# Kernel tuning notes

Measured on AMD Instinct MI355X. Metric: run time of the kernel, lower is better.

Reference implementation:

```python
import jax, jax.numpy as jnp
import numpy as np

B, N, D_IN = 128, 128, 1024
H1, D_OUT = 256, 32
K = 8  # num_clusters


def setup_inputs() -> dict:
    key = jax.random.key(0)
    ks = jax.random.split(key, 3)
    x = jax.random.normal(ks[0], (B, N, D_IN), dtype=jnp.float32)
    W1 = jax.random.normal(ks[1], (D_IN, H1), dtype=jnp.float32) * (1.0 / np.sqrt(D_IN))
    b1 = jnp.zeros((H1,), jnp.float32)
    W2 = jax.random.normal(ks[2], (H1, D_OUT), dtype=jnp.float32) * (1.0 / np.sqrt(H1))
    b2 = jnp.zeros((D_OUT,), jnp.float32)
    return {"x": x, "W1": W1, "b1": b1, "W2": W2, "b2": b2}


def _mlp(x, W1, b1, W2, b2):
    # nn.Sequential(GELU, Linear(1024,256), GELU, Linear(256,32)); torch GELU default = exact erf
    h = jax.nn.gelu(x, approximate=False)
    h = h @ W1 + b1
    h = jax.nn.gelu(h, approximate=False)
    return h @ W2 + b2  # [B, N, 32]


def _ward_labels(feats, k):
    """Greedy ward-linkage agglomerative clustering of feats [n, d] -> int labels [n].
    Ward merge cost d(A,B) = |A||B|/(|A|+|B|) * ||c_A - c_B||^2 (Lance-Williams equiv)."""
    n = feats.shape[0]
    eye = jnp.eye(n, dtype=bool)

    def body(t, state):
        cents, sizes, lab = state
        sq = jnp.sum(cents * cents, axis=-1)
        d2 = jnp.maximum(sq[:, None] + sq[None, :] - 2.0 * (cents @ cents.T), 0.0)
        w = (sizes[:, None] * sizes[None, :]) / (sizes[:, None] + sizes[None, :] + 1e-30)
        active = sizes > 0
        valid = (active[:, None] & active[None, :]) & (~eye)
        Dm = jnp.where(valid, w * d2, jnp.inf)
        idx = jnp.argmin(Dm)
        i, j = idx // n, idx % n
        i2 = jnp.minimum(i, j)
        j2 = jnp.maximum(i, j)
        si, sj = sizes[i2], sizes[j2]
        newc = (cents[i2] * si + cents[j2] * sj) / (si + sj)
        cents = cents.at[i2].set(newc)
        sizes = sizes.at[i2].set(si + sj).at[j2].set(0.0)
        lab = jnp.where(lab == j2, i2, lab)
        return cents, sizes, lab

    init = (feats, jnp.ones((n,), feats.dtype), jnp.arange(n))
    cents, sizes, lab = jax.lax.fori_loop(0, n - k, body, init)
    # relabel surviving representative indices to 0..k-1 (ordered by index)
    rank = jnp.cumsum((sizes > 0).astype(jnp.int32)) - 1
    return rank[lab]


def reference(x, W1, b1, W2, b2):
    feats = _mlp(x, W1, b1, W2, b2)          # [B, N, 32]
    labels = jax.vmap(lambda f: _ward_labels(f, K))(feats)  # [B, N] int32
    return labels
```

## Files before the change

### kernel.cpp

```cpp
#include <hip/hip_runtime.h>
#include <math.h>

#define BB 128
#define NN 128
#define DIN 1024
#define H1 256
#define DOUT 32
#define KCL 8
#define NPTS 128
#define MROWS (BB*NN)
#define CSTR 130
#define RSTR 132
#define HSTR 257
#define DEADKEY 0xFFFFFFFF00000000ull

__device__ __forceinline__ float gelu_exact(float v) {
    return 0.5f * v * (1.0f + erff(v * 0.70710678118654752f));
}

__device__ __forceinline__ unsigned long long mkkey(float v, int r, int j) {
    return ((unsigned long long)__float_as_uint(v) << 32) | (unsigned)((r << 7) | j);
}

__device__ __forceinline__ float readlanef(float v, int lane) {
    return __int_as_float(__builtin_amdgcn_readlane(__float_as_int(v), lane));
}

template<int CTRL, int RMASK>
__device__ __forceinline__ unsigned dpp_umin_step(unsigned v) {
    unsigned t = (unsigned)__builtin_amdgcn_update_dpp((int)v, (int)v, CTRL, RMASK, 0xf, false);
    return t < v ? t : v;
}
__device__ __forceinline__ unsigned wave_umin_bcast(unsigned v) {
    v = dpp_umin_step<0x111, 0xf>(v);
    v = dpp_umin_step<0x112, 0xf>(v);
    v = dpp_umin_step<0x114, 0xf>(v);
    v = dpp_umin_step<0x118, 0xf>(v);
    v = dpp_umin_step<0x142, 0xa>(v);
    v = dpp_umin_step<0x143, 0xc>(v);
    return (unsigned)__builtin_amdgcn_readlane((int)v, 63);
}
__device__ __forceinline__ unsigned half_umin(unsigned v) {
    v = dpp_umin_step<0x111, 0xf>(v);
    v = dpp_umin_step<0x112, 0xf>(v);
    v = dpp_umin_step<0x114, 0xf>(v);
    v = dpp_umin_step<0x118, 0xf>(v);
    v = dpp_umin_step<0x142, 0xa>(v);
    return v;
}

__global__ __launch_bounds__(256) void gelu_kernel(const float* __restrict__ x,
                                                   float* __restrict__ gx, int n4) {
    int i = blockIdx.x * 256 + threadIdx.x;
    const int stride = gridDim.x * 256;
    for (; i < n4; i += stride) {
        float4 v = ((const float4*)x)[i];
        v.x = gelu_exact(v.x);
        v.y = gelu_exact(v.y);
        v.z = gelu_exact(v.z);
        v.w = gelu_exact(v.w);
        ((float4*)gx)[i] = v;
    }
}

template<bool FUSE>
__global__ __launch_bounds__(256) void mlp1_kernel(const float* __restrict__ xin,
                                                   const float* __restrict__ W1,
                                                   const float* __restrict__ b1,
                                                   float* __restrict__ h) {
    __shared__ float As[64][68];
    __shared__ float Bs[64][68];
    const int bn = blockIdx.x;
    const int bm = blockIdx.y;
    const int tid = threadIdx.x;
    const int tx = tid & 15, ty = tid >> 4;

    float acc[4][4] = {{0.f}};

    const int arow = tid >> 2;
    const int kc   = (tid & 3) * 4;
    const int brow = tid >> 4;
    const int bcol4 = (tid & 15) * 4;

    const float* xrow = xin + (size_t)(bm * 64 + arow) * DIN;
    const float* wbase = W1 + bn * 64;

    for (int kt = 0; kt < DIN; kt += 64) {
        float4 a0 = *(const float4*)(xrow + kt + kc);
        float4 a1 = *(const float4*)(xrow + kt + kc + 16);
        float4 a2 = *(const float4*)(xrow + kt + kc + 32);
        float4 a3 = *(const float4*)(xrow + kt + kc + 48);
        float4 w0 = *(const float4*)(wbase + (size_t)(kt + brow) * H1 + bcol4);
        float4 w1 = *(const float4*)(wbase + (size_t)(kt + 16 + brow) * H1 + bcol4);
        float4 w2 = *(const float4*)(wbase + (size_t)(kt + 32 + brow) * H1 + bcol4);
        float4 w3 = *(const float4*)(wbase + (size_t)(kt + 48 + brow) * H1 + bcol4);
        __syncthreads();
        if (FUSE) {
            As[kc + 0][arow] = gelu_exact(a0.x);
            As[kc + 1][arow] = gelu_exact(a0.y);
            As[kc + 2][arow] = gelu_exact(a0.z);
            As[kc + 3][arow] = gelu_exact(a0.w);
            As[16 + kc + 0][arow] = gelu_exact(a1.x);
            As[16 + kc + 1][arow] = gelu_exact(a1.y);
            As[16 + kc + 2][arow] = gelu_exact(a1.z);
            As[16 + kc + 3][arow] = gelu_exact(a1.w);
            As[32 + kc + 0][arow] = gelu_exact(a2.x);
            As[32 + kc + 1][arow] = gelu_exact(a2.y);
            As[32 + kc + 2][arow] = gelu_exact(a2.z);
            As[32 + kc + 3][arow] = gelu_exact(a2.w);
            As[48 + kc + 0][arow] = gelu_exact(a3.x);
            As[48 + kc + 1][arow] = gelu_exact(a3.y);
            As[48 + kc + 2][arow] = gelu_exact(a3.z);
            As[48 + kc + 3][arow] = gelu_exact(a3.w);
        } else {
            As[kc + 0][arow] = a0.x;
            As[kc + 1][arow] = a0.y;
            As[kc + 2][arow] = a0.z;
            As[kc + 3][arow] = a0.w;
            As[16 + kc + 0][arow] = a1.x;
            As[16 + kc + 1][arow] = a1.y;
            As[16 + kc + 2][arow] = a1.z;
            As[16 + kc + 3][arow] = a1.w;
            As[32 + kc + 0][arow] = a2.x;
            As[32 + kc + 1][arow] = a2.y;
            As[32 + kc + 2][arow] = a2.z;
            As[32 + kc + 3][arow] = a2.w;
            As[48 + kc + 0][arow] = a3.x;
            As[48 + kc + 1][arow] = a3.y;
            As[48 + kc + 2][arow] = a3.z;
            As[48 + kc + 3][arow] = a3.w;
        }
        *(float4*)&Bs[brow][bcol4] = w0;
        *(float4*)&Bs[16 + brow][bcol4] = w1;
        *(float4*)&Bs[32 + brow][bcol4] = w2;
        *(float4*)&Bs[48 + brow][bcol4] = w3;
        __syncthreads();
#pragma unroll
        for (int kk = 0; kk < 64; ++kk) {
            float4 a = *(const float4*)&As[kk][ty * 4];
            float4 b = *(const float4*)&Bs[kk][tx * 4];
            float ar[4] = {a.x, a.y, a.z, a.w};
            float br[4] = {b.x, b.y, b.z, b.w};
#pragma unroll
            for (int i = 0; i < 4; ++i)
#pragma unroll
                for (int j = 0; j < 4; ++j)
                    acc[i][j] = fmaf(ar[i], br[j], acc[i][j]);
        }
    }

    const int row = bm * 64 + ty * 4;
    const int col = bn * 64 + tx * 4;
    float4 bias = *(const float4*)(b1 + col);
#pragma unroll
    for (int i = 0; i < 4; ++i) {
        float4 o;
        o.x = acc[i][0] + bias.x;
        o.y = acc[i][1] + bias.y;
        o.z = acc[i][2] + bias.z;
        o.w = acc[i][3] + bias.w;
        *(float4*)(h + (size_t)(row + i) * H1 + col) = o;
    }
}

__global__ __launch_bounds__(256) void mlp2_kernel(const float* __restrict__ h,
                                                   const float* __restrict__ W2,
                                                   const float* __restrict__ b2,
                                                   float* __restrict__ feats) {
    __shared__ float hs[32 * HSTR];
    __shared__ float w2s[H1 * DOUT];
    const int blk = blockIdx.x;
    const int tid = threadIdx.x;

    for (int i = tid; i < (H1 * DOUT) / 4; i += 256)
        ((float4*)w2s)[i] = ((const float4*)W2)[i];

    const float* hb = h + (size_t)blk * 32 * H1;
    const int sr = tid & 31;
    const int sk = (tid >> 5) * 32;
    const float* hrow = hb + (size_t)sr * H1 + sk;
#pragma unroll
    for (int j = 0; j < 8; ++j) {
        float4 v = ((const float4*)hrow)[j];
        hs[sr * HSTR + sk + 4 * j + 0] = gelu_exact(v.x);
        hs[sr * HSTR + sk + 4 * j + 1] = gelu_exact(v.y);
        hs[sr * HSTR + sk + 4 * j + 2] = gelu_exact(v.z);
        hs[sr * HSTR + sk + 4 * j + 3] = gelu_exact(v.w);
    }
    __syncthreads();

    const int row = tid >> 3;
    const int col4 = (tid & 7) * 4;
    const float4 bias = ((const float4*)b2)[tid & 7];
    float a0 = 0.f, a1 = 0.f, a2 = 0.f, a3 = 0.f;
    const float* hr = &hs[row * HSTR];
    for (int k = 0; k < H1; ++k) {
        float a = hr[k];
        float4 w = *(const float4*)&w2s[k * DOUT + col4];
        a0 = fmaf(a, w.x, a0);
        a1 = fmaf(a, w.y, a1);
        a2 = fmaf(a, w.z, a2);
        a3 = fmaf(a, w.w, a3);
    }
    float4 o;
    o.x = a0 + bias.x;
    o.y = a1 + bias.y;
    o.z = a2 + bias.z;
    o.w = a3 + bias.w;
    *(float4*)(feats + (size_t)(blk * 32 + row) * DOUT + col4) = o;
}

__global__ __launch_bounds__(256) void ward_kernel(const float* __restrict__ feats,
                                                   int* __restrict__ out) {
    __shared__ __align__(16) float cost[NPTS * RSTR];
    __shared__ __align__(16) float G[NPTS * RSTR];
    __shared__ float centsT[32 * CSTR];
    __shared__ unsigned long long rowkey[NPTS];
    __shared__ float sqArr[NPTS];
    __shared__ float szsE[NPTS];
    __shared__ int rnk[NPTS];

    const int b = blockIdx.x;
    const int tid = threadIdx.x;
    const float* f = feats + (size_t)b * NPTS * DOUT;
    const float INF = __builtin_inff();

    for (int i = tid; i < NPTS * DOUT; i += 256) {
        int r = i >> 5, d = i & 31;
        centsT[d * CSTR + r] = f[i];
    }
    __syncthreads();
    if (tid < NPTS) {
        float s = 0.f;
#pragma unroll
        for (int d = 0; d < 32; ++d) {
            float v = centsT[d * CSTR + tid];
            s = fmaf(v, v, s);
        }
        sqArr[tid] = s;
    }
    __syncthreads();
    {
        int ti = tid >> 4, tj = tid & 15;
        int I0 = ti * 8, J0 = tj * 8;
        float acc[8][8];
#pragma unroll
        for (int u = 0; u < 8; ++u)
#pragma unroll
            for (int v = 0; v < 8; ++v) acc[u][v] = 0.f;
        for (int d = 0; d < 32; ++d) {
            float a[8], bb[8];
#pragma unroll
            for (int u = 0; u < 8; ++u) a[u] = centsT[d * CSTR + I0 + u];
#pragma unroll
            for (int v = 0; v < 8; ++v) bb[v] = centsT[d * CSTR + J0 + v];
#pragma unroll
            for (int u = 0; u < 8; ++u)
#pragma unroll
                for (int v = 0; v < 8; ++v)
                    acc[u][v] = fmaf(a[u], bb[v], acc[u][v]);
        }
#pragma unroll
        for (int u = 0; u < 8; ++u) {
#pragma unroll
            for (int v = 0; v < 8; ++v) {
                int i = I0 + u, j = J0 + v;
                G[i * RSTR + j] = acc[u][v];
                float d2 = sqArr[i] + sqArr[j] - 2.0f * acc[u][v];
                if (d2 < 0.f) d2 = 0.f;
                float w = (1.0f * 1.0f) / (1.0f + 1.0f + 1e-30f);
                cost[i * RSTR + j] = (i == j) ? INF : w * d2;
            }
        }
    }
    __syncthreads();
    if (tid < NPTS) {
        unsigned long long best = DEADKEY;
        for (int j = 0; j < NPTS; ++j) {
            float v = cost[tid * RSTR + j];
            unsigned long long k = mkkey(v, tid, j);
            if (k < best) best = k;
        }
        rowkey[tid] = best;
    }
    __syncthreads();

    if (tid >= 64) return;
    const int lane = tid;
    const int hh = lane & 31;
    const int r0 = lane * 2, r1 = lane * 2 + 1;

    unsigned long long k0 = rowkey[r0], k1 = rowkey[r1];
    float q0 = sqArr[r0], q1 = sqArr[r1];
    float s0 = 1.0f, s1 = 1.0f;
    int lab0 = r0, lab1 = r1;
    unsigned long long alive0 = ~0ull, alive1 = ~0ull;

    for (int it = 0; it < NPTS - KCL; ++it) {
        unsigned bv0 = (unsigned)(k0 >> 32), bv1 = (unsigned)(k1 >> 32);
        unsigned lmin = bv0 < bv1 ? bv0 : bv1;
        unsigned lflat = (bv0 <= bv1) ? (unsigned)(k0 & 0x3FFFu) : (unsigned)(k1 & 0x3FFFu);
        unsigned gmin = wave_umin_bcast(lmin);
        unsigned long long bmask = __ballot(lmin == gmin);
        int lsel = __ffsll(bmask) - 1;
        unsigned flat = (unsigned)__builtin_amdgcn_readlane((int)lflat, lsel);
        int ra = (int)(flat >> 7), ca = (int)(flat & 127u);
        const int i2 = ra < ca ? ra : ca;
        const int j2 = ra < ca ? ca : ra;

        float2 gi = *(const float2*)&G[i2 * RSTR + r0];
        float2 gj = *(const float2*)&G[j2 * RSTR + r0];

        float si = readlanef((i2 & 1) ? s1 : s0, i2 >> 1);
        float sj = readlanef((j2 & 1) ? s1 : s0, j2 >> 1);
        const float snew = si + sj;
        const float invs = 1.0f / snew;
        const float wa = si * invs, wb = sj * invs;

        int arg0 = (int)(k0 & 127u), arg1 = (int)(k1 & 127u);
        bool d0 = (s0 > 0.f) && r0 != i2 && r0 != j2 && (arg0 == i2 || arg0 == j2);
        bool d1 = (s1 > 0.f) && r1 != i2 && r1 != j2 && (arg1 == i2 || arg1 == j2);
        unsigned long long m0 = __ballot(d0), m1 = __ballot(d1);

        float Gii = readlanef((i2 & 1) ? gi.y : gi.x, i2 >> 1);
        float Gij = readlanef((i2 & 1) ? gj.y : gj.x, i2 >> 1);
        float Gjj = readlanef((j2 & 1) ? gj.y : gj.x, j2 >> 1);
        float dotA = wa * Gii + wb * Gij;
        float dotB = wa * Gij + wb * Gjj;
        float qn = wa * dotA + wb * dotB;

        float dot0 = wa * gi.x + wb * gj.x;
        float dot1 = wa * gi.y + wb * gj.y;

        if (lab0 == j2) lab0 = i2;
        if (lab1 == j2) lab1 = i2;
        if (r0 == i2) s0 = snew; else if (r0 == j2) { s0 = 0.f; k0 = DEADKEY; }
        if (r1 == i2) s1 = snew; else if (r1 == j2) { s1 = 0.f; k1 = DEADKEY; }
        if (j2 < 64) alive0 &= ~(1ull << j2); else alive1 &= ~(1ull << (j2 - 64));
        if (r0 == i2) { dot0 = qn; q0 = qn; }
        if (r1 == i2) { dot1 = qn; q1 = qn; }

        *(float2*)&G[i2 * RSTR + r0] = make_float2(dot0, dot1);
        G[r0 * RSTR + i2] = dot0;
        G[r1 * RSTR + i2] = dot1;

        bool w0 = (s0 > 0.f) && r0 != i2 && r0 != j2;
        bool w1 = (s1 > 0.f) && r1 != i2 && r1 != j2;
        if (w0) {
            float d2 = q0 + qn - 2.0f * dot0;
            if (d2 < 0.f) d2 = 0.f;
            float w = (s0 * snew) / (s0 + snew + 1e-30f);
            float v0 = w * d2;
            cost[r0 * RSTR + i2] = v0;
            cost[i2 * RSTR + r0] = v0;
            if (!d0) {
                unsigned long long nk = mkkey(v0, r0, i2);
                if (nk < k0) k0 = nk;
            }
        }
        if (w1) {
            float d2 = q1 + qn - 2.0f * dot1;
            if (d2 < 0.f) d2 = 0.f;
            float w = (s1 * snew) / (s1 + snew + 1e-30f);
            float v1 = w * d2;
            cost[r1 * RSTR + i2] = v1;
            cost[i2 * RSTR + r1] = v1;
            if (!d1) {
                unsigned long long nk = mkkey(v1, r1, i2);
                if (nk < k1) k1 = nk;
            }
        }

        bool pi = true;
        unsigned long long mm0 = m0, mm1 = m1;
        while (pi | (mm0 != 0ull) | (mm1 != 0ull)) {
            int rA, rB;
            bool hasB = false;
            if (pi) { rA = i2; pi = false; }
            else if (mm0) { int t = __ffsll(mm0) - 1; rA = 2 * t; mm0 &= mm0 - 1; }
            else { int t = __ffsll(mm1) - 1; rA = 2 * t + 1; mm1 &= mm1 - 1; }
            if (mm0) { int t = __ffsll(mm0) - 1; rB = 2 * t; mm0 &= mm0 - 1; hasB = true; }
            else if (mm1) { int t = __ffsll(mm1) - 1; rB = 2 * t + 1; mm1 &= mm1 - 1; hasB = true; }
            else rB = rA;

            int r = (lane < 32) ? rA : rB;
            float4 cv = *(const float4*)&cost[r * RSTR + 4 * hh];
            unsigned long long word = (hh < 16) ? alive0 : alive1;
            unsigned nib = (unsigned)(word >> ((4 * hh) & 63)) & 0xFu;
            unsigned e0 = (nib & 1u) ? __float_as_uint(cv.x) : 0xFFFFFFFFu;
            unsigned e1 = (nib & 2u) ? __float_as_uint(cv.y) : 0xFFFFFFFFu;
            unsigned e2 = (nib & 4u) ? __float_as_uint(cv.z) : 0xFFFFFFFFu;
            unsigned e3 = (nib & 8u) ? __float_as_uint(cv.w) : 0xFFFFFFFFu;
            unsigned m = e0; int c = 0;
            if (e1 < m) { m = e1; c = 1; }
            if (e2 < m) { m = e2; c = 2; }
            if (e3 < m) { m = e3; c = 3; }
            int lcol = 4 * hh + c;
            unsigned hm = half_umin(m);
            unsigned vA = (unsigned)__builtin_amdgcn_readlane((int)hm, 31);
            unsigned vB = (unsigned)__builtin_amdgcn_readlane((int)hm, 63);
            unsigned vref = (lane < 32) ? vA : vB;
            unsigned long long msk = __ballot(m == vref);
            int laneA = __ffsll(msk & 0xFFFFFFFFull) - 1;
            int laneB = 32 + __ffsll(msk >> 32) - 1;
            int colA = __builtin_amdgcn_readlane(lcol, laneA);
            int colB = __builtin_amdgcn_readlane(lcol, laneB);
            unsigned long long keyA = ((unsigned long long)vA << 32) | (unsigned)((rA << 7) | colA);
            unsigned long long keyB = ((unsigned long long)vB << 32) | (unsigned)((rB << 7) | colB);
            if (lane == (rA >> 1)) { if (rA & 1) k1 = keyA; else k0 = keyA; }
            if (hasB && lane == (rB >> 1)) { if (rB & 1) k1 = keyB; else k0 = keyB; }
        }
    }

    szsE[r0] = s0;
    szsE[r1] = s1;
    __asm__ volatile("s_waitcnt lgkmcnt(0)" ::: "memory");
    if (lane == 0) {
        int c = 0;
        for (int i = 0; i < NPTS; ++i) rnk[i] = (szsE[i] > 0.f) ? c++ : -1;
    }
    __asm__ volatile("s_waitcnt lgkmcnt(0)" ::: "memory");
    out[b * NPTS + r0] = rnk[lab0];
    out[b * NPTS + r1] = rnk[lab1];
}

extern "C" void kernel_launch(void* const* d_in, const int* in_sizes, int n_in,
                              void* d_out, int out_size, void* d_ws, size_t ws_size,
                              hipStream_t stream) {
    const float* x  = (const float*)d_in[0];
    const float* W1 = (const float*)d_in[1];
    const float* b1 = (const float*)d_in[2];
    const float* W2 = (const float*)d_in[3];
    const float* b2 = (const float*)d_in[4];

    float* h = (float*)d_ws;
    float* feats = h + (size_t)MROWS * H1;
    float* gx = feats + (size_t)MROWS * DOUT;
    int* out = (int*)d_out;

    const size_t need = ((size_t)MROWS * H1 + (size_t)MROWS * DOUT + (size_t)MROWS * DIN) * 4;
    const bool use_gx = ws_size >= need;

    if (use_gx) {
        gelu_kernel<<<2048, 256, 0, stream>>>(x, gx, MROWS * DIN / 4);
        mlp1_kernel<false><<<dim3(H1 / 64, MROWS / 64), 256, 0, stream>>>(gx, W1, b1, h);
    } else {
        mlp1_kernel<true><<<dim3(H1 / 64, MROWS / 64), 256, 0, stream>>>(x, W1, b1, h);
    }
    mlp2_kernel<<<MROWS / 32, 256, 0, stream>>>(h, W2, b2, feats);
    ward_kernel<<<BB, 256, 0, stream>>>(feats, out);
}
```

Measured before the change: 427.3 us.

## Swizzle G/cost LDS columns and load W1 tiles via global_load_lds

Stores the Gram and cost matrices in LDS with a per-row rotated column layout (rotation by 4*((row>>1)&31)) so that column-wise accesses in the merge loop spread across banks rather than colliding. Every index into G and cost is remapped to match, including the alive-mask nibble lookup and the recovered column index in the row-min scan. Separately, the W1 tile in the MLP GEMM is copied straight from global memory into LDS with the global_load_lds builtin, dropping the register staging and the row padding. The remapping is fiddly and any index error would silently give wrong labels; the direct-to-LDS load also changes how the B-tile fill overlaps with the A-tile writes.

```diff
diff --git a/kernel.cpp b/kernel.cpp
--- a/kernel.cpp
+++ b/kernel.cpp
@@ -69,7 +69,7 @@
                                                    const float* __restrict__ b1,
                                                    float* __restrict__ h) {
     __shared__ float As[64][68];
-    __shared__ float Bs[64][68];
+    __shared__ float Bs[64][64];
     const int bn = blockIdx.x;
     const int bm = blockIdx.y;
     const int tid = threadIdx.x;
@@ -79,8 +79,10 @@
 
     const int arow = tid >> 2;
     const int kc   = (tid & 3) * 4;
-    const int brow = tid >> 4;
-    const int bcol4 = (tid & 15) * 4;
+    const int wv   = tid >> 6;
+    const int ln   = tid & 63;
+    const int bkr  = ln >> 4;
+    const int bkc  = (ln & 15) * 4;
 
     const float* xrow = xin + (size_t)(bm * 64 + arow) * DIN;
     const float* wbase = W1 + bn * 64;
@@ -90,11 +92,15 @@
         float4 a1 = *(const float4*)(xrow + kt + kc + 16);
         float4 a2 = *(const float4*)(xrow + kt + kc + 32);
         float4 a3 = *(const float4*)(xrow + kt + kc + 48);
-        float4 w0 = *(const float4*)(wbase + (size_t)(kt + brow) * H1 + bcol4);
-        float4 w1 = *(const float4*)(wbase + (size_t)(kt + 16 + brow) * H1 + bcol4);
-        float4 w2 = *(const float4*)(wbase + (size_t)(kt + 32 + brow) * H1 + bcol4);
-        float4 w3 = *(const float4*)(wbase + (size_t)(kt + 48 + brow) * H1 + bcol4);
         __syncthreads();
+#pragma unroll
+        for (int s = 0; s < 4; ++s) {
+            const int kr = wv * 16 + s * 4;
+            const float* g = wbase + (size_t)(kt + kr + bkr) * H1 + bkc;
+            __builtin_amdgcn_global_load_lds(
+                (const __attribute__((address_space(1))) unsigned int*)g,
+                (__attribute__((address_space(3))) unsigned int*)&Bs[kr][0], 16, 0, 0);
+        }
         if (FUSE) {
             As[kc + 0][arow] = gelu_exact(a0.x);
             As[kc + 1][arow] = gelu_exact(a0.y);
@@ -130,10 +136,6 @@
             As[48 + kc + 2][arow] = a3.z;
             As[48 + kc + 3][arow] = a3.w;
         }
-        *(float4*)&Bs[brow][bcol4] = w0;
-        *(float4*)&Bs[16 + brow][bcol4] = w1;
-        *(float4*)&Bs[32 + brow][bcol4] = w2;
-        *(float4*)&Bs[48 + brow][bcol4] = w3;
         __syncthreads();
 #pragma unroll
         for (int kk = 0; kk < 64; ++kk) {
@@ -262,22 +264,26 @@
         }
 #pragma unroll
         for (int u = 0; u < 8; ++u) {
+            const int i = I0 + u;
+            const int rq = 4 * ((i >> 1) & 31);
 #pragma unroll
             for (int v = 0; v < 8; ++v) {
-                int i = I0 + u, j = J0 + v;
-                G[i * RSTR + j] = acc[u][v];
+                int j = J0 + v;
+                int pc = (j + rq) & 127;
+                G[i * RSTR + pc] = acc[u][v];
                 float d2 = sqArr[i] + sqArr[j] - 2.0f * acc[u][v];
                 if (d2 < 0.f) d2 = 0.f;
                 float w = (1.0f * 1.0f) / (1.0f + 1.0f + 1e-30f);
-                cost[i * RSTR + j] = (i == j) ? INF : w * d2;
+                cost[i * RSTR + pc] = (i == j) ? INF : w * d2;
             }
         }
     }
     __syncthreads();
     if (tid < NPTS) {
         unsigned long long best = DEADKEY;
+        const int rq = 4 * ((tid >> 1) & 31);
         for (int j = 0; j < NPTS; ++j) {
-            float v = cost[tid * RSTR + j];
+            float v = cost[tid * RSTR + ((j + rq) & 127)];
             unsigned long long k = mkkey(v, tid, j);
             if (k < best) best = k;
         }
@@ -289,6 +295,7 @@
     const int lane = tid;
     const int hh = lane & 31;
     const int r0 = lane * 2, r1 = lane * 2 + 1;
+    const int hq4 = 4 * hh;
 
     unsigned long long k0 = rowkey[r0], k1 = rowkey[r1];
     float q0 = sqArr[r0], q1 = sqArr[r1];
@@ -307,9 +314,11 @@
         int ra = (int)(flat >> 7), ca = (int)(flat & 127u);
         const int i2 = ra < ca ? ra : ca;
         const int j2 = ra < ca ? ca : ra;
-
-        float2 gi = *(const float2*)&G[i2 * RSTR + r0];
-        float2 gj = *(const float2*)&G[j2 * RSTR + r0];
+        const int ri2 = 4 * ((i2 >> 1) & 31);
+        const int rj2 = 4 * ((j2 >> 1) & 31);
+
+        float2 gi = *(const float2*)&G[i2 * RSTR + ((r0 + ri2) & 127)];
+        float2 gj = *(const float2*)&G[j2 * RSTR + ((r0 + rj2) & 127)];
 
         float si = readlanef((i2 & 1) ? s1 : s0, i2 >> 1);
         float sj = readlanef((j2 & 1) ? s1 : s0, j2 >> 1);
@@ -340,9 +349,9 @@
         if (r0 == i2) { dot0 = qn; q0 = qn; }
         if (r1 == i2) { dot1 = qn; q1 = qn; }
 
-        *(float2*)&G[i2 * RSTR + r0] = make_float2(dot0, dot1);
-        G[r0 * RSTR + i2] = dot0;
-        G[r1 * RSTR + i2] = dot1;
+        *(float2*)&G[i2 * RSTR + ((r0 + ri2) & 127)] = make_float2(dot0, dot1);
+        G[r0 * RSTR + ((i2 + hq4) & 127)] = dot0;
+        G[r1 * RSTR + ((i2 + hq4) & 127)] = dot1;
 
         bool w0 = (s0 > 0.f) && r0 != i2 && r0 != j2;
         bool w1 = (s1 > 0.f) && r1 != i2 && r1 != j2;
@@ -351,8 +360,8 @@
             if (d2 < 0.f) d2 = 0.f;
             float w = (s0 * snew) / (s0 + snew + 1e-30f);
             float v0 = w * d2;
-            cost[r0 * RSTR + i2] = v0;
-            cost[i2 * RSTR + r0] = v0;
+            cost[r0 * RSTR + ((i2 + hq4) & 127)] = v0;
+            cost[i2 * RSTR + ((r0 + ri2) & 127)] = v0;
             if (!d0) {
                 unsigned long long nk = mkkey(v0, r0, i2);
                 if (nk < k0) k0 = nk;
@@ -363,8 +372,8 @@
             if (d2 < 0.f) d2 = 0.f;
             float w = (s1 * snew) / (s1 + snew + 1e-30f);
             float v1 = w * d2;
-            cost[r1 * RSTR + i2] = v1;
-            cost[i2 * RSTR + r1] = v1;
+            cost[r1 * RSTR + ((i2 + hq4) & 127)] = v1;
+            cost[i2 * RSTR + ((r1 + ri2) & 127)] = v1;
             if (!d1) {
                 unsigned long long nk = mkkey(v1, r1, i2);
                 if (nk < k1) k1 = nk;
@@ -385,8 +394,9 @@
 
             int r = (lane < 32) ? rA : rB;
             float4 cv = *(const float4*)&cost[r * RSTR + 4 * hh];
-            unsigned long long word = (hh < 16) ? alive0 : alive1;
-            unsigned nib = (unsigned)(word >> ((4 * hh) & 63)) & 0xFu;
+            int lq = (hh - ((r >> 1) & 31)) & 31;
+            unsigned long long word = (lq < 16) ? alive0 : alive1;
+            unsigned nib = (unsigned)(word >> ((4 * lq) & 63)) & 0xFu;
             unsigned e0 = (nib & 1u) ? __float_as_uint(cv.x) : 0xFFFFFFFFu;
             unsigned e1 = (nib & 2u) ? __float_as_uint(cv.y) : 0xFFFFFFFFu;
             unsigned e2 = (nib & 4u) ? __float_as_uint(cv.z) : 0xFFFFFFFFu;
@@ -395,7 +405,7 @@
             if (e1 < m) { m = e1; c = 1; }
             if (e2 < m) { m = e2; c = 2; }
             if (e3 < m) { m = e3; c = 3; }
-            int lcol = 4 * hh + c;
+            int lcol = 4 * lq + c;
             unsigned hm = half_umin(m);
             unsigned vA = (unsigned)__builtin_amdgcn_readlane((int)hm, 31);
             unsigned vB = (unsigned)__builtin_amdgcn_readlane((int)hm, 63);
```

Result: slower. 446.1 us (+4.4%).
